# Optimization experiments

Hardware: AMD Instinct MI355X
Metric: run time of the kernel (lower is better)

Reference implementation:

```python
import jax, jax.numpy as jnp
import numpy as np

B, S, DIM = 1, 2048, 4096
NH, NKV, HD = 32, 8, 128  # n_head, n_local_heads (kv heads), head_dim
ROPE_BASE = 10000.0


def setup_inputs() -> dict:
    key = jax.random.key(0)
    k1, k2, k3 = jax.random.split(key, 3)
    x = jax.random.normal(k1, (B, S, DIM), dtype=jnp.float32)
    total_head_dim = (NH + 2 * NKV) * HD  # 6144
    wqkv = jax.random.normal(k2, (total_head_dim, DIM), dtype=jnp.float32) * 0.02
    wo = jax.random.normal(k3, (DIM, DIM), dtype=jnp.float32) * 0.02
    # standard RoPE table: (S, HD//2, 2) = (cos, sin)
    inv_freq = 1.0 / (ROPE_BASE ** (np.arange(0, HD, 2, dtype=np.float32) / HD))
    ang = np.outer(np.arange(S, dtype=np.float32), inv_freq)
    freqs_cis = jnp.asarray(np.stack([np.cos(ang), np.sin(ang)], axis=-1), dtype=jnp.float32)
    return {"x": x, "freqs_cis": freqs_cis, "wqkv": wqkv, "wo": wo}


def _apply_rotary(x, freqs_cis):
    # x: (b, s, h, d); freqs_cis: (s, d//2, 2)
    b, s, h, d = x.shape
    xs = x.reshape(b, s, h, d // 2, 2)
    fc = freqs_cis.reshape(1, s, 1, d // 2, 2)
    re = xs[..., 0] * fc[..., 0] - xs[..., 1] * fc[..., 1]
    im = xs[..., 0] * fc[..., 1] + xs[..., 1] * fc[..., 0]
    return jnp.stack([re, im], axis=-1).reshape(b, s, h, d)


def reference(x, freqs_cis, wqkv, wo):
    b, s, _ = x.shape
    kv_size = NKV * HD
    qkv = x @ wqkv.T  # (b, s, (NH+2*NKV)*HD)
    q, k, v = jnp.split(qkv, [NH * HD, NH * HD + kv_size], axis=-1)
    q = q.reshape(b, s, NH, HD)
    k = k.reshape(b, s, NKV, HD)
    v = v.reshape(b, s, NKV, HD)
    q = _apply_rotary(q, freqs_cis)
    k = _apply_rotary(k, freqs_cis)
    rep = NH // NKV  # GQA expansion factor; repeat_kv == grouped einsum below
    qg = q.reshape(b, s, NKV, rep, HD)
    scale = 1.0 / jnp.sqrt(jnp.asarray(HD, q.dtype))
    # scores: (b, g, r, q_pos, k_pos) -- avoids materializing repeated K/V
    scores = jnp.einsum('bqgrd,bkgd->bgrqk', qg, k) * scale
    causal = jnp.tril(jnp.ones((s, s), dtype=bool))
    scores = jnp.where(causal, scores, jnp.finfo(scores.dtype).min)
    p = jax.nn.softmax(scores, axis=-1)
    o = jnp.einsum('bgrqk,bkgd->bqgrd', p, v).reshape(b, s, NH * HD)
    return o @ wo.T
```

## Files before the change

### kernel.cpp

```cpp
#include <hip/hip_runtime.h>
#include <hip/hip_bf16.h>
#include <math.h>


typedef __attribute__((ext_vector_type(8))) __bf16 bf16x8;
typedef __attribute__((ext_vector_type(4))) __bf16 bf16x4;
typedef __attribute__((ext_vector_type(4))) float f32x4;

#define NEG_BIG (-1e30f)

#define ASYNC_CP16(gsrc, ldst)                                                            \
  __builtin_amdgcn_global_load_lds((const __attribute__((address_space(1))) void*)(gsrc), \
                                   (__attribute__((address_space(3))) void*)(ldst), 16, 0, 0)

__device__ __forceinline__ f32x4 mfma_bf16(bf16x8 a, bf16x8 b, f32x4 c) {
  return __builtin_amdgcn_mfma_f32_16x16x32_bf16(a, b, c, 0, 0, 0);
}

__device__ __forceinline__ float clampf(float v) {
  return fminf(fmaxf(v, -30000.f), 30000.f);
}

__device__ __forceinline__ bf16x8 ldg8(const __hip_bfloat16* p) {
  return *(const bf16x8*)p;
}
__device__ __forceinline__ bf16x8 ldg8(const float* p) {
  f32x4 a = *(const f32x4*)p;
  f32x4 b = *(const f32x4*)(p + 4);
  bf16x8 r;
  r[0] = (__bf16)a[0]; r[1] = (__bf16)a[1]; r[2] = (__bf16)a[2]; r[3] = (__bf16)a[3];
  r[4] = (__bf16)b[0]; r[5] = (__bf16)b[1]; r[6] = (__bf16)b[2]; r[7] = (__bf16)b[3];
  return r;
}

__device__ __forceinline__ void store_c(float* C, size_t idx, float v) {
  C[idx] = clampf(v);
}
__device__ __forceinline__ void store_c(__hip_bfloat16* C, size_t idx, float v) {
  C[idx] = __float2bfloat16(clampf(v));
}

__global__ __launch_bounds__(256) void cvt_f32_bf16(const float* __restrict__ src,
                                                    __hip_bfloat16* __restrict__ dst) {
  size_t i = ((size_t)blockIdx.x * 256 + threadIdx.x) * 8;
  *(bf16x8*)&dst[i] = ldg8(src + i);
}

__global__ __launch_bounds__(256) void gemm_qkv_rope(
    const __hip_bfloat16* __restrict__ A, const __hip_bfloat16* __restrict__ B,
    __hip_bfloat16* __restrict__ qkv, __hip_bfloat16* __restrict__ vt,
    const float* __restrict__ fc) {
  const int K = 4096;
  __shared__ __align__(16) __hip_bfloat16 As[128 * 32];
  __shared__ __align__(16) __hip_bfloat16 Bs[128 * 32];
  const int tid = threadIdx.x;
  const int lane = tid & 63, wave = tid >> 6;
  const int l15 = lane & 15, quad = lane >> 4;
  const int wm = (wave >> 1) * 64, wn = (wave & 1) * 64;
  const size_t mBase = (size_t)blockIdx.y * 128, nBase = (size_t)blockIdx.x * 128;

  const int ldRow = tid >> 2;
  const int ldCol = (tid & 3) * 8;
  const __hip_bfloat16* Ap = A + (mBase + ldRow) * (size_t)K + ldCol;
  const __hip_bfloat16* Bp = B + (nBase + ldRow) * (size_t)K + ldCol;

  f32x4 acc[4][4] = {};

  for (int k0 = 0; k0 < K; k0 += 32) {
    ASYNC_CP16(Ap, &As[tid * 8]);
    ASYNC_CP16(Ap + (size_t)64 * K, &As[2048 + tid * 8]);
    ASYNC_CP16(Bp, &Bs[tid * 8]);
    ASYNC_CP16(Bp + (size_t)64 * K, &Bs[2048 + tid * 8]);
    Ap += 32; Bp += 32;
    __syncthreads();
    bf16x8 af[4], bfr[4];
#pragma unroll
    for (int i = 0; i < 4; i++)
      af[i] = *(const bf16x8*)&As[(wm + i * 16 + l15) * 32 + quad * 8];
#pragma unroll
    for (int j = 0; j < 4; j++)
      bfr[j] = *(const bf16x8*)&Bs[(wn + j * 16 + l15) * 32 + quad * 8];
#pragma unroll
    for (int i = 0; i < 4; i++)
#pragma unroll
      for (int j = 0; j < 4; j++)
        acc[i][j] = mfma_bf16(af[i], bfr[j], acc[i][j]);
    __syncthreads();
  }

#pragma unroll
  for (int i = 0; i < 4; i++)
#pragma unroll
    for (int j = 0; j < 4; j++) {
      size_t c = nBase + wn + j * 16 + l15;
      size_t srow0 = mBase + wm + i * 16 + quad * 4;
      if (c < 5120) {
        int di2 = (int)(c & 126);
#pragma unroll
        for (int r = 0; r < 4; r++) {
          float v = clampf(acc[i][j][r]);
          float vp = __shfl_xor(v, 1);
          size_t s = srow0 + r;
          float cs = fc[s * 128 + di2];
          float sn = fc[s * 128 + di2 + 1];
          float ov = ((c & 1) == 0) ? (v * cs - vp * sn) : (vp * sn + v * cs);
          qkv[s * 6144 + c] = __float2bfloat16(ov);
        }
      } else {
        bf16x4 pk;
#pragma unroll
        for (int r = 0; r < 4; r++) pk[r] = (__bf16)clampf(acc[i][j][r]);
        *(bf16x4*)&vt[(c - 5120) * 2048 + srow0] = pk;
      }
    }
}

template <typename TC>
__global__ __launch_bounds__(256) void gemm_nt_async(
    const __hip_bfloat16* __restrict__ A, const __hip_bfloat16* __restrict__ B,
    TC* __restrict__ C, int M, int N, int K) {
  __shared__ __align__(16) __hip_bfloat16 As[128 * 32];
  __shared__ __align__(16) __hip_bfloat16 Bs[128 * 32];
  const int tid = threadIdx.x;
  const int lane = tid & 63, wave = tid >> 6;
  const int l15 = lane & 15, quad = lane >> 4;
  const int wm = (wave >> 1) * 64, wn = (wave & 1) * 64;
  const size_t mBase = (size_t)blockIdx.y * 128, nBase = (size_t)blockIdx.x * 128;

  const int ldRow = tid >> 2;
  const int ldCol = (tid & 3) * 8;
  const __hip_bfloat16* Ap = A + (mBase + ldRow) * (size_t)K + ldCol;
  const __hip_bfloat16* Bp = B + (nBase + ldRow) * (size_t)K + ldCol;

  f32x4 acc[4][4] = {};

  for (int k0 = 0; k0 < K; k0 += 32) {
    ASYNC_CP16(Ap, &As[tid * 8]);
    ASYNC_CP16(Ap + (size_t)64 * K, &As[2048 + tid * 8]);
    ASYNC_CP16(Bp, &Bs[tid * 8]);
    ASYNC_CP16(Bp + (size_t)64 * K, &Bs[2048 + tid * 8]);
    Ap += 32; Bp += 32;
    __syncthreads();
    bf16x8 af[4], bfr[4];
#pragma unroll
    for (int i = 0; i < 4; i++)
      af[i] = *(const bf16x8*)&As[(wm + i * 16 + l15) * 32 + quad * 8];
#pragma unroll
    for (int j = 0; j < 4; j++)
      bfr[j] = *(const bf16x8*)&Bs[(wn + j * 16 + l15) * 32 + quad * 8];
#pragma unroll
    for (int i = 0; i < 4; i++)
#pragma unroll
      for (int j = 0; j < 4; j++)
        acc[i][j] = mfma_bf16(af[i], bfr[j], acc[i][j]);
    __syncthreads();
  }

#pragma unroll
  for (int i = 0; i < 4; i++)
#pragma unroll
    for (int j = 0; j < 4; j++)
#pragma unroll
      for (int r = 0; r < 4; r++) {
        size_t row = mBase + wm + i * 16 + quad * 4 + r;
        size_t col = nBase + wn + j * 16 + l15;
        store_c(C, row * (size_t)N + col, acc[i][j][r]);
      }
}

template <typename TA, typename TB, typename TC>
__global__ __launch_bounds__(256) void gemm_nt(
    const TA* __restrict__ A, const TB* __restrict__ B,
    TC* __restrict__ C, int M, int N, int K) {
  __shared__ __align__(16) __hip_bfloat16 As[128 * 32];
  __shared__ __align__(16) __hip_bfloat16 Bs[128 * 32];
  const int tid = threadIdx.x;
  const int lane = tid & 63, wave = tid >> 6;
  const int l15 = lane & 15, quad = lane >> 4;
  const int wm = (wave >> 1) * 64, wn = (wave & 1) * 64;
  const size_t mBase = (size_t)blockIdx.y * 128, nBase = (size_t)blockIdx.x * 128;
  const int ldRow = tid >> 2;
  const int ldCol = (tid & 3) * 8;
  const TA* Ap = A + (mBase + ldRow) * (size_t)K + ldCol;
  const TB* Bp = B + (nBase + ldRow) * (size_t)K + ldCol;
  f32x4 acc[4][4] = {};
  for (int k0 = 0; k0 < K; k0 += 32) {
    bf16x8 a0 = ldg8(Ap);
    bf16x8 a1 = ldg8(Ap + (size_t)64 * K);
    bf16x8 b0 = ldg8(Bp);
    bf16x8 b1 = ldg8(Bp + (size_t)64 * K);
    Ap += 32; Bp += 32;
    *(bf16x8*)&As[tid * 8] = a0;
    *(bf16x8*)&As[2048 + tid * 8] = a1;
    *(bf16x8*)&Bs[tid * 8] = b0;
    *(bf16x8*)&Bs[2048 + tid * 8] = b1;
    __syncthreads();
    bf16x8 af[4], bfr[4];
#pragma unroll
    for (int i = 0; i < 4; i++)
      af[i] = *(const bf16x8*)&As[(wm + i * 16 + l15) * 32 + quad * 8];
#pragma unroll
    for (int j = 0; j < 4; j++)
      bfr[j] = *(const bf16x8*)&Bs[(wn + j * 16 + l15) * 32 + quad * 8];
#pragma unroll
    for (int i = 0; i < 4; i++)
#pragma unroll
      for (int j = 0; j < 4; j++)
        acc[i][j] = mfma_bf16(af[i], bfr[j], acc[i][j]);
    __syncthreads();
  }
#pragma unroll
  for (int i = 0; i < 4; i++)
#pragma unroll
    for (int j = 0; j < 4; j++)
#pragma unroll
      for (int r = 0; r < 4; r++) {
        size_t row = mBase + wm + i * 16 + quad * 4 + r;
        size_t col = nBase + wn + j * 16 + l15;
        store_c(C, row * (size_t)N + col, acc[i][j][r]);
      }
}

__global__ __launch_bounds__(256) void rope_kernel(__hip_bfloat16* __restrict__ qkv,
                                                   const float* __restrict__ fc) {
  int idx = blockIdx.x * 256 + threadIdx.x;
  int d = idx & 63;
  int h = (idx >> 6) % 40;
  int s = idx / (40 * 64);
  size_t off = (size_t)s * 6144 + h * 128 + d * 2;
  float x0 = __bfloat162float(qkv[off]);
  float x1 = __bfloat162float(qkv[off + 1]);
  float c = fc[s * 128 + d * 2];
  float sn = fc[s * 128 + d * 2 + 1];
  qkv[off] = __float2bfloat16(x0 * c - x1 * sn);
  qkv[off + 1] = __float2bfloat16(x0 * sn + x1 * c);
}

__global__ __launch_bounds__(256) void transpose_v(const __hip_bfloat16* __restrict__ qkv,
                                                   __hip_bfloat16* __restrict__ vt) {
  __shared__ __hip_bfloat16 tile[32][33];
  int x = threadIdx.x & 31, y = threadIdx.x >> 5;
  int colBase = blockIdx.x * 32;
  int sBase = blockIdx.y * 32;
#pragma unroll
  for (int i = 0; i < 4; i++)
    tile[y + i * 8][x] = qkv[(size_t)(sBase + y + i * 8) * 6144 + 5120 + colBase + x];
  __syncthreads();
#pragma unroll
  for (int i = 0; i < 4; i++)
    vt[(size_t)(colBase + y + i * 8) * 2048 + sBase + x] = tile[x][y + i * 8];
}

__global__ __launch_bounds__(256) void flash_attn(
    const __hip_bfloat16* __restrict__ qkv, const __hip_bfloat16* __restrict__ vt,
    __hip_bfloat16* __restrict__ o) {
  __shared__ __align__(16) __hip_bfloat16 Ks[64 * 128];
  __shared__ __align__(16) __hip_bfloat16 Vs[128 * 64];
  __shared__ __align__(16) __hip_bfloat16 Ps[4][16 * 72];
  const int tid = threadIdx.x;
  const int lane = tid & 63, wave = tid >> 6;
  const int l15 = lane & 15, quad = lane >> 4;
  const int h = blockIdx.x, g = h >> 2;
  const int qt = 15 - blockIdx.y;
  const int qBase = qt * 128;
  const int qRowW = qBase + wave * 32;

  bf16x8 qf[2][4];
#pragma unroll
  for (int t = 0; t < 2; t++) {
    const __hip_bfloat16* qp =
        qkv + (size_t)(qRowW + t * 16 + l15) * 6144 + h * 128 + quad * 8;
#pragma unroll
    for (int d = 0; d < 4; d++) qf[t][d] = *(const bf16x8*)(qp + d * 32);
  }

  f32x4 acc_o[2][8] = {};
  float m_i[2][4], l_i[2][4];
#pragma unroll
  for (int t = 0; t < 2; t++)
#pragma unroll
    for (int r = 0; r < 4; r++) { m_i[t][r] = NEG_BIG; l_i[t][r] = 0.f; }

  const float scale = 0.08838834764831845f;
  const int nkt = 2 * qt + 2;
  for (int kt = 0; kt < nkt; kt++) {
    const int kBase = kt * 64;
#pragma unroll
    for (int rnd = 0; rnd < 4; rnd++) {
      int ci = rnd * 256 + tid;
      int row = ci >> 4, chl = ci & 15;
      int chg = chl ^ (row & 15);
      ASYNC_CP16(qkv + (size_t)(kBase + row) * 6144 + 4096 + g * 128 + chg * 8, &Ks[ci * 8]);
    }
#pragma unroll
    for (int rnd = 0; rnd < 4; rnd++) {
      int ci = rnd * 256 + tid;
      int n = ci >> 3, chl = ci & 7;
      int chg = chl ^ (n & 7);
      ASYNC_CP16(vt + (size_t)(g * 128 + n) * 2048 + kBase + chg * 8, &Vs[ci * 8]);
    }
    __syncthreads();

    f32x4 sc[2][4] = {};
#pragma unroll
    for (int d = 0; d < 4; d++) {
#pragma unroll
      for (int j = 0; j < 4; j++) {
        bf16x8 kb = *(const bf16x8*)&Ks[(j * 16 + l15) * 128 + ((d * 4 + quad) ^ l15) * 8];
        sc[0][j] = mfma_bf16(qf[0][d], kb, sc[0][j]);
        sc[1][j] = mfma_bf16(qf[1][d], kb, sc[1][j]);
      }
    }

#pragma unroll
    for (int t = 0; t < 2; t++) {
      const int qRowT = qRowW + t * 16;
      float rowmax[4] = {NEG_BIG, NEG_BIG, NEG_BIG, NEG_BIG};
      float sv[4][4];
#pragma unroll
      for (int j = 0; j < 4; j++) {
        int kcol = kBase + j * 16 + l15;
#pragma unroll
        for (int r = 0; r < 4; r++) {
          float s = clampf(sc[t][j][r] * scale);
          if (kcol > qRowT + quad * 4 + r) s = NEG_BIG;
          sv[j][r] = s;
          rowmax[r] = fmaxf(rowmax[r], s);
        }
      }
#pragma unroll
      for (int off = 8; off; off >>= 1)
#pragma unroll
        for (int r = 0; r < 4; r++)
          rowmax[r] = fmaxf(rowmax[r], __shfl_xor(rowmax[r], off, 16));

      float alpha[4], rowsum[4];
#pragma unroll
      for (int r = 0; r < 4; r++) {
        float mnew = fmaxf(m_i[t][r], rowmax[r]);
        alpha[r] = __expf(m_i[t][r] - mnew);
        m_i[t][r] = mnew;
        rowsum[r] = 0.f;
      }
#pragma unroll
      for (int j = 0; j < 4; j++)
#pragma unroll
        for (int r = 0; r < 4; r++) {
          float p = __expf(sv[j][r] - m_i[t][r]);
          rowsum[r] += p;
          Ps[wave][(quad * 4 + r) * 72 + j * 16 + l15] = __float2bfloat16(p);
        }
#pragma unroll
      for (int off = 8; off; off >>= 1)
#pragma unroll
        for (int r = 0; r < 4; r++)
          rowsum[r] += __shfl_xor(rowsum[r], off, 16);
#pragma unroll
      for (int r = 0; r < 4; r++) l_i[t][r] = l_i[t][r] * alpha[r] + rowsum[r];

#pragma unroll
      for (int jt = 0; jt < 8; jt++)
#pragma unroll
        for (int r = 0; r < 4; r++) acc_o[t][jt][r] *= alpha[r];

#pragma unroll
      for (int kk = 0; kk < 2; kk++) {
        bf16x8 pa = *(const bf16x8*)&Ps[wave][l15 * 72 + kk * 32 + quad * 8];
#pragma unroll
        for (int jt = 0; jt < 8; jt++) {
          int n = jt * 16 + l15;
          bf16x8 vb = *(const bf16x8*)&Vs[n * 64 + (((kk * 4 + quad) ^ (n & 7))) * 8];
          acc_o[t][jt] = mfma_bf16(pa, vb, acc_o[t][jt]);
        }
      }
    }
    __syncthreads();
  }

#pragma unroll
  for (int t = 0; t < 2; t++)
#pragma unroll
    for (int r = 0; r < 4; r++) {
      float inv = 1.f / l_i[t][r];
      size_t qr = qRowW + t * 16 + quad * 4 + r;
#pragma unroll
      for (int jt = 0; jt < 8; jt++)
        o[qr * 4096 + h * 128 + jt * 16 + l15] =
            __float2bfloat16(clampf(acc_o[t][jt][r] * inv));
    }
}

extern "C" void kernel_launch(void* const* d_in, const int* in_sizes, int n_in,
                              void* d_out, int out_size, void* d_ws, size_t ws_size,
                              hipStream_t stream) {
  const float* x = (const float*)d_in[0];
  const float* fc = (const float*)d_in[1];
  const float* wqkv = (const float*)d_in[2];
  const float* wo = (const float*)d_in[3];
  float* out = (float*)d_out;

  char* ws = (char*)d_ws;
  __hip_bfloat16* qkv = (__hip_bfloat16*)ws;
  __hip_bfloat16* vt  = (__hip_bfloat16*)(ws + 25165824);
  __hip_bfloat16* ob  = (__hip_bfloat16*)(ws + 29360128);
  __hip_bfloat16* xb  = (__hip_bfloat16*)(ws + 46137344);
  __hip_bfloat16* wb  = (__hip_bfloat16*)(ws + 62914560);

  const bool fast = ws_size >= (size_t)113246208;

  if (fast) {
    cvt_f32_bf16<<<dim3(4096), 256, 0, stream>>>(x, xb);
    cvt_f32_bf16<<<dim3(12288), 256, 0, stream>>>(wqkv, wb);
    gemm_qkv_rope<<<dim3(48, 16), 256, 0, stream>>>(xb, wb, qkv, vt, fc);
  } else {
    gemm_nt<float, float, __hip_bfloat16>
        <<<dim3(48, 16), 256, 0, stream>>>(x, wqkv, qkv, 2048, 6144, 4096);
    rope_kernel<<<dim3(20480), 256, 0, stream>>>(qkv, fc);
    transpose_v<<<dim3(32, 64), 256, 0, stream>>>(qkv, vt);
  }
  flash_attn<<<dim3(32, 16), 256, 0, stream>>>(qkv, vt, ob);
  if (fast) {
    cvt_f32_bf16<<<dim3(8192), 256, 0, stream>>>(wo, wb);
    gemm_nt_async<float>
        <<<dim3(32, 16), 256, 0, stream>>>(ob, wb, out, 2048, 4096, 4096);
  } else {
    gemm_nt<__hip_bfloat16, float, float>
        <<<dim3(32, 16), 256, 0, stream>>>(ob, wo, out, 2048, 4096, 4096);
  }
}
```

Before: 550.0 us.

## Rewrite QKV GEMM with 256x256 tiles, double-buffered swizzled LDS pipeline

The fused QKV+RoPE GEMM moves from 128x128 tiles with 4 waves and a single synchronous LDS buffer to 256x256 tiles with 8 waves. Global-to-LDS async copies are double-buffered over a BK=64 stage and interleaved with the MFMA phases, gated by explicit vmcnt waits and split barriers. LDS reads use an XOR swizzle to avoid bank conflicts, and setprio raises the priority of MFMA issue. The goal is to hide load latency and raise arithmetic intensity, at the cost of 128KB LDS per block and a grid of only 192 blocks, which may leave some CUs idle.

```diff
diff --git a/kernel.cpp b/kernel.cpp
--- a/kernel.cpp
+++ b/kernel.cpp
@@ -40,60 +40,130 @@
   C[idx] = __float2bfloat16(clampf(v));
 }
 
+__device__ __forceinline__ void barrier_np() {
+  asm volatile("" ::: "memory");
+  __builtin_amdgcn_s_barrier();
+  asm volatile("" ::: "memory");
+}
+
 __global__ __launch_bounds__(256) void cvt_f32_bf16(const float* __restrict__ src,
                                                     __hip_bfloat16* __restrict__ dst) {
   size_t i = ((size_t)blockIdx.x * 256 + threadIdx.x) * 8;
   *(bf16x8*)&dst[i] = ldg8(src + i);
 }
 
-__global__ __launch_bounds__(256) void gemm_qkv_rope(
+__global__ __launch_bounds__(512, 2) void gemm_qkv_rope(
     const __hip_bfloat16* __restrict__ A, const __hip_bfloat16* __restrict__ B,
     __hip_bfloat16* __restrict__ qkv, __hip_bfloat16* __restrict__ vt,
     const float* __restrict__ fc) {
-  const int K = 4096;
-  __shared__ __align__(16) __hip_bfloat16 As[128 * 32];
-  __shared__ __align__(16) __hip_bfloat16 Bs[128 * 32];
+  const int NT = 64;
+  __shared__ __align__(16) __hip_bfloat16 lds[4][16384];
+  __hip_bfloat16* const As0 = lds[0];
+  __hip_bfloat16* const Bs0 = lds[1];
+  __hip_bfloat16* const As1 = lds[2];
+  __hip_bfloat16* const Bs1 = lds[3];
+
   const int tid = threadIdx.x;
-  const int lane = tid & 63, wave = tid >> 6;
+  const int lane = tid & 63, wid = tid >> 6;
   const int l15 = lane & 15, quad = lane >> 4;
-  const int wm = (wave >> 1) * 64, wn = (wave & 1) * 64;
-  const size_t mBase = (size_t)blockIdx.y * 128, nBase = (size_t)blockIdx.x * 128;
-
-  const int ldRow = tid >> 2;
-  const int ldCol = (tid & 3) * 8;
-  const __hip_bfloat16* Ap = A + (mBase + ldRow) * (size_t)K + ldCol;
-  const __hip_bfloat16* Bp = B + (nBase + ldRow) * (size_t)K + ldCol;
-
-  f32x4 acc[4][4] = {};
-
-  for (int k0 = 0; k0 < K; k0 += 32) {
-    ASYNC_CP16(Ap, &As[tid * 8]);
-    ASYNC_CP16(Ap + (size_t)64 * K, &As[2048 + tid * 8]);
-    ASYNC_CP16(Bp, &Bs[tid * 8]);
-    ASYNC_CP16(Bp + (size_t)64 * K, &Bs[2048 + tid * 8]);
-    Ap += 32; Bp += 32;
-    __syncthreads();
-    bf16x8 af[4], bfr[4];
-#pragma unroll
-    for (int i = 0; i < 4; i++)
-      af[i] = *(const bf16x8*)&As[(wm + i * 16 + l15) * 32 + quad * 8];
-#pragma unroll
-    for (int j = 0; j < 4; j++)
-      bfr[j] = *(const bf16x8*)&Bs[(wn + j * 16 + l15) * 32 + quad * 8];
-#pragma unroll
-    for (int i = 0; i < 4; i++)
-#pragma unroll
-      for (int j = 0; j < 4; j++)
-        acc[i][j] = mfma_bf16(af[i], bfr[j], acc[i][j]);
-    __syncthreads();
-  }
-
-#pragma unroll
-  for (int i = 0; i < 4; i++)
-#pragma unroll
-    for (int j = 0; j < 4; j++) {
-      size_t c = nBase + wn + j * 16 + l15;
-      size_t srow0 = mBase + wm + i * 16 + quad * 4;
+  const int wr = wid >> 2, wc = wid & 3;
+  const size_t mBase = (size_t)blockIdx.y * 256, nBase = (size_t)blockIdx.x * 256;
+
+  const int rdOff = l15 * 64 + ((quad * 16) ^ ((l15 & 8) << 2));
+  const int wr8 = wr * 8;
+  const int wc4 = wc * 4;
+
+  const char* pAsrc[4];
+  const char* pBsrc[4];
+  int LAel[4], LBel[4];
+#pragma unroll
+  for (int u = 0; u < 4; ++u) {
+    int LA = (tid < 256) ? (4096 * u + tid * 16) : (16384 + 4096 * u + (tid - 256) * 16);
+    int LAs = LA ^ (((LA >> 9) & 1) << 5);
+    int stA = LAs >> 10, rA16 = (LAs >> 6) & 15, cbA = LAs & 63;
+    int rowA = (stA >> 1) * 16 + rA16;
+    int colA = (stA & 1) * 32 + (cbA >> 1);
+    pAsrc[u] = (const char*)A + ((mBase + rowA) * (size_t)4096 + colA) * 2;
+    LAel[u] = LA >> 1;
+
+    int LB = u * 8192 + tid * 16;
+    int LBs = LB ^ (((LB >> 9) & 1) << 5);
+    int stB = LBs >> 10, rB16 = (LBs >> 6) & 15, cbB = LBs & 63;
+    int rowB = (stB >> 1) * 16 + rB16;
+    int colB = (stB & 1) * 32 + (cbB >> 1);
+    pBsrc[u] = (const char*)B + ((nBase + rowB) * (size_t)4096 + colB) * 2;
+    LBel[u] = LB >> 1;
+  }
+
+  f32x4 acc[8][4] = {};
+
+#pragma unroll
+  for (int u = 0; u < 4; ++u) {
+    ASYNC_CP16(pAsrc[u], As0 + LAel[u]);
+    ASYNC_CP16(pBsrc[u], Bs0 + LBel[u]);
+  }
+#pragma unroll
+  for (int u = 0; u < 3; ++u) {
+    ASYNC_CP16(pAsrc[u] + 128, As1 + LAel[u]);
+    ASYNC_CP16(pBsrc[u] + 128, Bs1 + LBel[u]);
+  }
+  asm volatile("s_waitcnt vmcnt(6)" ::: "memory");
+  barrier_np();
+
+#define QKV_TILE(tt, CA, CB, AA, AB)                                                     \
+  {                                                                                      \
+    bf16x8 bfr[4][2];                                                                    \
+    _Pragma("unroll") for (int p = 0; p < 4; ++p) {                                      \
+      bf16x8 afr[2][2];                                                                  \
+      _Pragma("unroll") for (int ii = 0; ii < 2; ++ii)                                   \
+          _Pragma("unroll") for (int kk = 0; kk < 2; ++kk)                               \
+              afr[ii][kk] = *(const bf16x8*)((const char*)(CA) +                         \
+                                             ((wr8 + 2 * p + ii) * 2048 + kk * 1024 + rdOff)); \
+      if (p == 0) {                                                                      \
+        _Pragma("unroll") for (int j = 0; j < 4; ++j)                                    \
+            _Pragma("unroll") for (int kk = 0; kk < 2; ++kk)                             \
+                bfr[j][kk] = *(const bf16x8*)((const char*)(CB) +                        \
+                                              ((wc4 + j) * 2048 + kk * 1024 + rdOff));   \
+        if ((tt) + 1 < NT) {                                                             \
+          ASYNC_CP16(pAsrc[3] + ((tt) + 1) * 128, (AA) + LAel[3]);                       \
+          ASYNC_CP16(pBsrc[3] + ((tt) + 1) * 128, (AB) + LBel[3]);                       \
+        }                                                                                \
+      } else if ((tt) + 2 < NT) {                                                        \
+        ASYNC_CP16(pAsrc[p - 1] + ((tt) + 2) * 128, (CA) + LAel[p - 1]);                 \
+        ASYNC_CP16(pBsrc[p - 1] + ((tt) + 2) * 128, (CB) + LBel[p - 1]);                 \
+      }                                                                                  \
+      barrier_np();                                                                      \
+      asm volatile("s_waitcnt lgkmcnt(0)" ::: "memory");                                 \
+      __builtin_amdgcn_sched_barrier(0);                                                 \
+      __builtin_amdgcn_s_setprio(1);                                                     \
+      _Pragma("unroll") for (int ii = 0; ii < 2; ++ii)                                   \
+          _Pragma("unroll") for (int j = 0; j < 4; ++j)                                  \
+              _Pragma("unroll") for (int kk = 0; kk < 2; ++kk)                           \
+                  acc[2 * p + ii][j] = mfma_bf16(afr[ii][kk], bfr[j][kk], acc[2 * p + ii][j]); \
+      __builtin_amdgcn_s_setprio(0);                                                     \
+      if (p == 3) {                                                                      \
+        if ((tt) < NT - 2) {                                                             \
+          asm volatile("s_waitcnt vmcnt(6)" ::: "memory");                               \
+        } else if ((tt) == NT - 2) {                                                     \
+          asm volatile("s_waitcnt vmcnt(0)" ::: "memory");                               \
+        }                                                                                \
+      }                                                                                  \
+      barrier_np();                                                                      \
+    }                                                                                    \
+  }
+
+  for (int t2 = 0; t2 < NT; t2 += 2) {
+    QKV_TILE(t2, As0, Bs0, As1, Bs1);
+    QKV_TILE(t2 + 1, As1, Bs1, As0, Bs0);
+  }
+#undef QKV_TILE
+
+#pragma unroll
+  for (int i = 0; i < 8; ++i)
+#pragma unroll
+    for (int j = 0; j < 4; ++j) {
+      size_t c = nBase + wc * 64 + j * 16 + l15;
+      size_t srow0 = mBase + wr * 128 + i * 16 + quad * 4;
       if (c < 5120) {
         int di2 = (int)(c & 126);
 #pragma unroll
@@ -411,7 +481,7 @@
   if (fast) {
     cvt_f32_bf16<<<dim3(4096), 256, 0, stream>>>(x, xb);
     cvt_f32_bf16<<<dim3(12288), 256, 0, stream>>>(wqkv, wb);
-    gemm_qkv_rope<<<dim3(48, 16), 256, 0, stream>>>(xb, wb, qkv, vt, fc);
+    gemm_qkv_rope<<<dim3(24, 8), 512, 0, stream>>>(xb, wb, qkv, vt, fc);
   } else {
     gemm_nt<float, float, __hip_bfloat16>
         <<<dim3(48, 16), 256, 0, stream>>>(x, wqkv, qkv, 2048, 6144, 4096);
```

Measured after the change: 552.7 us. Within noise of the previous version (+0.5%).
